# Kernel tuning notes

Measured on AMD Instinct MI355X. Metric: run time of the kernel, lower is better.

## Reference

```python
import jax, jax.numpy as jnp
import numpy as np

N0, N1, N2 = 100000, 300000, 150000
P = 2
DIM = 64


def spmm(rows, cols, vals, dense, n_rows):
    # sparse[n_rows, n_cols] @ dense[n_cols, d] via gather + segment_sum
    return jax.ops.segment_sum(vals[:, None] * dense[cols], rows, num_segments=n_rows)


def powcat(X, p):
    # torch.cat([X**1, ..., X**p], dim=1)
    return jnp.concatenate([X ** n for n in range(1, p + 1)], axis=1)


def setup_inputs() -> dict:
    key = jax.random.key(0)
    ks = iter(jax.random.split(key, 64))

    def randn(shape, scale=1.0):
        return jax.random.normal(next(ks), shape, dtype=jnp.float32) * scale

    def sparse(nr, nc, nnz):
        r = jax.random.randint(next(ks), (nnz,), 0, nr, dtype=jnp.int32)
        c = jax.random.randint(next(ks), (nnz,), 0, nc, dtype=jnp.int32)
        v = randn((nnz,), 0.1)
        return r, c, v

    inp = {}
    inp["X0"] = randn((N0, DIM))
    inp["X1"] = randn((N1, DIM))
    inp["X2"] = randn((N2, DIM))
    for name, nr, nc, nnz in [
        ("L0", N0, N0, 1000000),
        ("L1", N1, N1, 2400000),
        ("L2", N2, N2, 1200000),
        ("D1invB1", N0, N1, 600000),
        ("D2B1TD1inv", N1, N0, 600000),
        ("B2TD2inv", N2, N1, 450000),
        ("B2D3", N1, N2, 450000),
    ]:
        r, c, v = sparse(nr, nc, nnz)
        inp[name + "_rows"], inp[name + "_cols"], inp[name + "_vals"] = r, c, v
    wscale = 1.0 / np.sqrt(DIM * P)
    for name in ["n2n", "n2e", "e2e", "e2n", "e2t", "t2e", "t2t"]:
        inp["W_" + name] = randn((DIM * P, DIM), wscale)
        inp["b_" + name] = randn((DIM,), wscale)
    return inp


def reference(X0, X1, X2,
              L0_rows, L0_cols, L0_vals,
              L1_rows, L1_cols, L1_vals,
              L2_rows, L2_cols, L2_vals,
              D1invB1_rows, D1invB1_cols, D1invB1_vals,
              D2B1TD1inv_rows, D2B1TD1inv_cols, D2B1TD1inv_vals,
              B2TD2inv_rows, B2TD2inv_cols, B2TD2inv_vals,
              B2D3_rows, B2D3_cols, B2D3_vals,
              W_n2n, b_n2n, W_n2e, b_n2e, W_e2e, b_e2e, W_e2n, b_e2n,
              W_e2t, b_e2t, W_t2e, b_t2e, W_t2t, b_t2t):
    X0c = powcat(X0, P)  # [N0, 2*d]
    X1c = powcat(X1, P)  # [N1, 2*d]
    X2c = powcat(X2, P)  # [N2, 2*d]

    n2n = spmm(L0_rows, L0_cols, L0_vals, X0c @ W_n2n + b_n2n, N0)
    n2e = spmm(D2B1TD1inv_rows, D2B1TD1inv_cols, D2B1TD1inv_vals, X0c @ W_n2e + b_n2e, N1)
    e2n = spmm(D1invB1_rows, D1invB1_cols, D1invB1_vals, X1c @ W_e2n + b_e2n, N0)
    e2e = spmm(L1_rows, L1_cols, L1_vals, X1c @ W_e2e + b_e2e, N1)
    e2t = spmm(B2TD2inv_rows, B2TD2inv_cols, B2TD2inv_vals, X1c @ W_e2t + b_e2t, N2)
    t2t = spmm(L2_rows, L2_cols, L2_vals, X2c @ W_t2t + b_t2t, N2)
    t2e = spmm(B2D3_rows, B2D3_cols, B2D3_vals, X2c @ W_t2e + b_t2e, N1)

    Y0 = 0.5 * jax.nn.relu(n2n + e2n)
    Y1 = (1.0 / 3.0) * jax.nn.relu(e2e + n2e + t2e)
    Y2 = 0.5 * jax.nn.relu(t2t + e2t)
    return (Y0, Y1, Y2)
```

## Files before the change

### kernel.cpp

```cpp
#include <hip/hip_runtime.h>
#include <hip/hip_bf16.h>


#define RPB 128
#define COL_MASK 0x7FFFFu
#define LROW_SH 19
#define DID_SH 26
#define CCOL_MASK 0x1FFFFFu
#define CLROW_SH 21
#define CBKT_SH 28
#define MAXNB 4352
#define GBK 4
#define GSH 2
#define NBIN 512
#define MAXNG 1088
#define GRID_BIN 256
#define SPMM_GRID 2048

#define CAPS        15744
#define SORT_PH     8192
#define SORT_LOG    13
#define SORT_MAXBIN 7552
#define MAXPH 16

typedef __attribute__((ext_vector_type(8))) short short8;
typedef __attribute__((ext_vector_type(4))) float f32x4;

__device__ __forceinline__ int   ntld_i(const int* p)   { return __builtin_nontemporal_load(p); }
__device__ __forceinline__ float ntld_f(const float* p) { return __builtin_nontemporal_load(p); }
__device__ __forceinline__ float4 ntld_f4(const float* p) {
    const unsigned long long* q = (const unsigned long long*)p;
    unsigned long long a = __builtin_nontemporal_load(q);
    unsigned long long b = __builtin_nontemporal_load(q + 1);
    float4 v;
    v.x = __uint_as_float((unsigned)a);
    v.y = __uint_as_float((unsigned)(a >> 32));
    v.z = __uint_as_float((unsigned)b);
    v.w = __uint_as_float((unsigned)(b >> 32));
    return v;
}
__device__ __forceinline__ void ntst_f4(float* p, float4 v) {
    unsigned long long a = (unsigned long long)__float_as_uint(v.x)
                         | ((unsigned long long)__float_as_uint(v.y) << 32);
    unsigned long long b = (unsigned long long)__float_as_uint(v.z)
                         | ((unsigned long long)__float_as_uint(v.w) << 32);
    unsigned long long* q = (unsigned long long*)p;
    __builtin_nontemporal_store(a, q);
    __builtin_nontemporal_store(b, q + 1);
}

__device__ __forceinline__ unsigned short f2bf(float f) {
    unsigned u = __float_as_uint(f);
    unsigned r = u + 0x7FFFu + ((u >> 16) & 1u);
    return (unsigned short)(r >> 16);
}

__device__ __forceinline__ void split8(float4 a0, float4 a1, short8& hi, short8& lo) {
    float v[8] = {a0.x, a0.y, a0.z, a0.w, a1.x, a1.y, a1.z, a1.w};
    #pragma unroll
    for (int e = 0; e < 8; ++e) {
        unsigned short h = f2bf(v[e]);
        float hf = __uint_as_float((unsigned)h << 16);
        hi[e] = (short)h;
        lo[e] = (short)f2bf(v[e] - hf);
    }
}

struct WAll { const float* w[7]; };

__global__ __launch_bounds__(256) void winit(WAll wa, unsigned short* __restrict__ frags)
{
    const int s = blockIdx.x;
    const float* __restrict__ W = wa.w[s];
    unsigned short* __restrict__ out = frags + (size_t)s * 16384;
    for (int slot = threadIdx.x; slot < 1024; slot += 256) {
        const int l  = slot & 63;
        const int nf = (slot >> 6) & 3;
        const int kk = slot >> 8;
        const int col = nf * 16 + (l & 15);
        const int kb  = kk * 32 + 8 * (l >> 4);
        short8 vh, vl;
        #pragma unroll
        for (int e = 0; e < 8; ++e) {
            float w = W[(size_t)(kb + e) * 64 + col];
            unsigned short h = f2bf(w);
            float hf = __uint_as_float((unsigned)h << 16);
            vh[e] = (short)h;
            vl[e] = (short)f2bf(w - hf);
        }
        *(short8*)(out + ((size_t)((kk * 4 + nf) * 2 + 0) * 64 + l) * 8) = vh;
        *(short8*)(out + ((size_t)((kk * 4 + nf) * 2 + 1) * 64 + l) * 8) = vl;
    }
}

__device__ __forceinline__ void mfma_set(
    const short8 Ah[4], const short8 Al[4],
    const unsigned short* __restrict__ F, const float* __restrict__ bias,
    unsigned short* __restrict__ D, int nrows, int row0w, int l)
{
    const int lg = l >> 4, lr = l & 15;
    const short8* __restrict__ Fv = (const short8*)F;
    f32x4 acc[4];
    #pragma unroll
    for (int nf = 0; nf < 4; ++nf) {
        float b = bias[nf * 16 + lr];
        f32x4 bi = {b, b, b, b};
        acc[nf] = bi;
    }
    #pragma unroll
    for (int kk = 0; kk < 4; ++kk) {
        #pragma unroll
        for (int nf = 0; nf < 4; ++nf) {
            short8 bh = Fv[((kk * 4 + nf) * 2 + 0) * 64 + l];
            short8 bl = Fv[((kk * 4 + nf) * 2 + 1) * 64 + l];
            acc[nf] = __builtin_amdgcn_mfma_f32_16x16x32_bf16(Ah[kk], bh, acc[nf], 0, 0, 0);
            acc[nf] = __builtin_amdgcn_mfma_f32_16x16x32_bf16(Al[kk], bh, acc[nf], 0, 0, 0);
            acc[nf] = __builtin_amdgcn_mfma_f32_16x16x32_bf16(Ah[kk], bl, acc[nf], 0, 0, 0);
        }
    }
    #pragma unroll
    for (int nf = 0; nf < 4; ++nf) {
        #pragma unroll
        for (int j = 0; j < 4; ++j) {
            int row = row0w + lg * 4 + j;
            if (row < nrows)
                D[(size_t)row * 64 + nf * 16 + lr] = f2bf(acc[nf][j]);
        }
    }
}

__device__ __forceinline__ void gemm_body(
    const float* __restrict__ X, int nrows, int nsets, int row0,
    const unsigned short* F0, const float* b0, unsigned short* D0,
    const unsigned short* F1, const float* b1, unsigned short* D1,
    const unsigned short* F2, const float* b2, unsigned short* D2,
    float Xs[64][68])
{
    const int tid = threadIdx.x;
    #pragma unroll
    for (int it = 0; it < 4; ++it) {
        int idx = tid + it * 256;
        int r = idx >> 4, c4 = idx & 15;
        float4 v = make_float4(0.f, 0.f, 0.f, 0.f);
        if (row0 + r < nrows)
            v = ntld_f4(X + (size_t)(row0 + r) * 64 + c4 * 4);
        *(float4*)&Xs[r][c4 * 4] = v;
    }
    __syncthreads();

    const int w = tid >> 6, l = tid & 63;
    const int lg = l >> 4, lr = l & 15;

    short8 Ah[4], Al[4];
    #pragma unroll
    for (int kk = 0; kk < 4; ++kk) {
        const float* p = &Xs[w * 16 + lr][(kk & 1) * 32 + 8 * lg];
        float4 a0 = *(const float4*)p;
        float4 a1 = *(const float4*)(p + 4);
        if (kk >= 2) {
            a0.x *= a0.x; a0.y *= a0.y; a0.z *= a0.z; a0.w *= a0.w;
            a1.x *= a1.x; a1.y *= a1.y; a1.z *= a1.z; a1.w *= a1.w;
        }
        split8(a0, a1, Ah[kk], Al[kk]);
    }

    const int row0w = row0 + w * 16;
    mfma_set(Ah, Al, F0, b0, D0, nrows, row0w, l);
    if (nsets > 1) mfma_set(Ah, Al, F1, b1, D1, nrows, row0w, l);
    if (nsets > 2) mfma_set(Ah, Al, F2, b2, D2, nrows, row0w, l);
}

__global__ __launch_bounds__(256) void gemm_powcat_mfma(
    const float* __restrict__ X, int nrows, int nsets,
    const unsigned short* __restrict__ F0, const float* __restrict__ b0, unsigned short* __restrict__ D0,
    const unsigned short* __restrict__ F1, const float* __restrict__ b1, unsigned short* __restrict__ D1,
    const unsigned short* __restrict__ F2, const float* __restrict__ b2, unsigned short* __restrict__ D2)
{
    __shared__ float Xs[64][68];
    gemm_body(X, nrows, nsets, blockIdx.x * 64,
              F0, b0, D0, F1, b1, D1, F2, b2, D2, Xs);
}

struct GemmJob {
    const float* X[3];
    const unsigned short* F[9];
    const float* bias[9];
    unsigned short* D[9];
    int nrows[3];
    int nsets[3];
    int blk0[4];
};

__global__ __launch_bounds__(256) void gemm_powcat_all(GemmJob J)
{
    __shared__ float Xs[64][68];
    const int bid = blockIdx.x;
    const int s = (bid >= J.blk0[1] ? 1 : 0) + (bid >= J.blk0[2] ? 1 : 0);
    const int row0 = (bid - J.blk0[s]) * 64;
    gemm_body(J.X[s], J.nrows[s], J.nsets[s], row0,
              J.F[s*3+0], J.bias[s*3+0], J.D[s*3+0],
              J.F[s*3+1], J.bias[s*3+1], J.D[s*3+1],
              J.F[s*3+2], J.bias[s*3+2], J.D[s*3+2], Xs);
}

struct Bin7 {
    const int *r0, *r1, *r2, *r3, *r4, *r5, *r6;
    const int *c0, *c1, *c2, *c3, *c4, *c5, *c6;
    const float *v0, *v1, *v2, *v3, *v4, *v5, *v6;
    int p1, p2, p3, p4, p5, p6, p7;
    int t0, t1, t2, t3, t4, t5, t6;
};

struct CBase { int b[8]; };

struct Ent { int r; int tb; unsigned cw; float v; };

template<bool FULL>
__device__ __forceinline__ Ent decode(const Bin7& B, int i) {
    Ent e;
    if (i < B.p1) {
        int li = i;
        e.r = ntld_i(B.r0 + li); e.tb = B.t0;
        if (FULL) { e.cw = (unsigned)ntld_i(B.c0 + li) | (0u << DID_SH); e.v = ntld_f(B.v0 + li); }
    } else if (i < B.p2) {
        int li = i - B.p1;
        e.r = ntld_i(B.r1 + li); e.tb = B.t1;
        if (FULL) { e.cw = (unsigned)ntld_i(B.c1 + li) | (1u << DID_SH); e.v = ntld_f(B.v1 + li); }
    } else if (i < B.p3) {
        int li = i - B.p2;
        e.r = ntld_i(B.r2 + li); e.tb = B.t2;
        if (FULL) { e.cw = (unsigned)ntld_i(B.c2 + li) | (2u << DID_SH); e.v = ntld_f(B.v2 + li); }
    } else if (i < B.p4) {
        int li = i - B.p3;
        e.r = ntld_i(B.r3 + li); e.tb = B.t3;
        if (FULL) { e.cw = (unsigned)ntld_i(B.c3 + li) | (3u << DID_SH); e.v = ntld_f(B.v3 + li); }
    } else if (i < B.p5) {
        int li = i - B.p4;
        e.r = ntld_i(B.r4 + li); e.tb = B.t4;
        if (FULL) { e.cw = (unsigned)ntld_i(B.c4 + li) | (4u << DID_SH); e.v = ntld_f(B.v4 + li); }
    } else if (i < B.p6) {
        int li = i - B.p5;
        e.r = ntld_i(B.r5 + li); e.tb = B.t5;
        if (FULL) { e.cw = (unsigned)ntld_i(B.c5 + li) | (5u << DID_SH); e.v = ntld_f(B.v5 + li); }
    } else {
        int li = i - B.p6;
        e.r = ntld_i(B.r6 + li); e.tb = B.t6;
        if (FULL) { e.cw = (unsigned)ntld_i(B.c6 + li) | (6u << DID_SH); e.v = ntld_f(B.v6 + li); }
    }
    return e;
}

__global__ __launch_bounds__(1024) void bhist_grp(
    Bin7 B, int* __restrict__ gcount, int* __restrict__ ghist,
    int NG, int chunk)
{
    __shared__ int h[MAXNG];
    for (int i = threadIdx.x; i < NG; i += 1024) h[i] = 0;
    __syncthreads();
    const int s = blockIdx.x * chunk;
    int e = s + chunk;  if (e > B.p7) e = B.p7;
    for (int i = s + threadIdx.x; i < e; i += 1024) {
        Ent en = decode<false>(B, i);
        atomicAdd(&h[(en.tb + (en.r >> 7)) >> GSH], 1);
    }
    __syncthreads();
    for (int i = threadIdx.x; i < NG; i += 1024) {
        int c = h[i];
        ghist[(size_t)blockIdx.x * NG + i] = c;
        if (c) atomicAdd(&gcount[i], c);
    }
}

__global__ __launch_bounds__(1024) void scatter_grpC(
    Bin7 B, CBase cb, int* __restrict__ gcur, const int* __restrict__ ghist,
    uint2* __restrict__ payA, int NG, int chunk)
{
    __shared__ int lbase[MAXNG];
    __shared__ int lcur[MAXNG];
    __shared__ int cbs[8];
    if (threadIdx.x < 8) cbs[threadIdx.x] = cb.b[threadIdx.x];
    for (int i = threadIdx.x; i < NG; i += 1024) {
        int c = ghist[(size_t)blockIdx.x * NG + i];
        lbase[i] = c ? atomicAdd(&gcur[i], c) : 0;
        lcur[i] = 0;
    }
    __syncthreads();
    const int s = blockIdx.x * chunk;
    int e = s + chunk;  if (e > B.p7) e = B.p7;
    for (int i = s + threadIdx.x; i < e; i += 1024) {
        Ent en = decode<true>(B, i);
        int b = en.tb + (en.r >> 7);
        int g = b >> GSH;
        int pos = lbase[g] + atomicAdd(&lcur[g], 1);
        int did = (int)(en.cw >> DID_SH);
        unsigned colC = (en.cw & COL_MASK) + (unsigned)cbs[did];
        unsigned cwA = colC | ((unsigned)(en.r & 127) << CLROW_SH)
                     | ((unsigned)(b & (GBK - 1)) << CBKT_SH);
        payA[pos] = make_uint2(cwA, __float_as_uint(en.v));
    }
}

__global__ __launch_bounds__(1024) void sort_grpC(
    const uint2* __restrict__ payA, const int* __restrict__ goff,
    const int* __restrict__ gcur, int* __restrict__ rowoff,
    int* __restrict__ bend, uint2* __restrict__ payB,
    unsigned char* __restrict__ rowperm, int NBtot)
{
    __shared__ uint2 lpay[CAPS];
    __shared__ unsigned short sidx[CAPS];
    __shared__ int cnt[NBIN];
    __shared__ int off[NBIN];
    __shared__ unsigned char cnts8[NBIN];
    __shared__ int wsum[8];
    __shared__ int phstart[MAXPH + 1];
    __shared__ int s_nph, s_maxbin;

    const int g = blockIdx.x;
    const int tid = threadIdx.x;
    const int seg0 = goff[g], seg1 = gcur[g];
    const int n = seg1 - seg0;
    const bool fast = (n <= CAPS);

    if (tid < NBIN) cnt[tid] = 0;
    if (tid == 0) s_maxbin = 0;
    __syncthreads();
    for (int i = seg0 + tid; i < seg1; i += 1024) {
        unsigned long long pv = __builtin_nontemporal_load(
            (const unsigned long long*)(payA + i));
        unsigned w = (unsigned)pv;
        if (fast) lpay[i - seg0] = make_uint2(w, (unsigned)(pv >> 32));
        atomicAdd(&cnt[(w >> CLROW_SH) & (NBIN - 1)], 1);
    }
    __syncthreads();

    const int lane = tid & 63, wv = tid >> 6;
    const int tot = (tid < NBIN) ? cnt[tid] : 0;
    if (tid < NBIN) {
        atomicMax(&s_maxbin, tot);
        cnts8[tid] = (unsigned char)(tot > 255 ? 255 : tot);
    }
    int x = tot;
    #pragma unroll
    for (int o = 1; o < 64; o <<= 1) {
        int y = __shfl_up(x, o);
        if (lane >= o) x += y;
    }
    if (lane == 63 && wv < 8) wsum[wv] = x;
    __syncthreads();
    if (tid == 0) {
        int acc = 0;
        #pragma unroll
        for (int j = 0; j < 8; ++j) { int t = wsum[j]; wsum[j] = acc; acc += t; }
    }
    __syncthreads();
    int excl = 0;
    if (tid < NBIN) {
        excl = (x - tot) + wsum[wv];
        off[tid] = excl;
        rowoff[(size_t)g * NBIN + tid] = seg0 + excl;
        int b = g * GBK + (tid >> 7);
        if (b < NBtot && (tid & 127) == 127) bend[b] = seg0 + excl + tot;
    }
    __syncthreads();
    if (tid < NBIN) {
        cnt[tid] = excl;
        int p = excl >> SORT_LOG;
        int pprev = (tid == 0) ? -1 : (off[tid - 1] >> SORT_LOG);
        for (int q = pprev + 1; q <= p && q <= MAXPH; ++q) phstart[q] = excl;
        if (tid == NBIN - 1) s_nph = p + 1;
        const int myr = tid & 127, b0 = tid & ~127;
        const unsigned char myc = cnts8[tid];
        int rank = 0;
        #pragma unroll 8
        for (int r = 0; r < 128; ++r) {
            unsigned char c = cnts8[b0 + r];
            rank += (c > myc) || (c == myc && r < myr);
        }
        rowperm[(size_t)g * NBIN + b0 + rank] = (unsigned char)myr;
    }
    __syncthreads();

    if (n <= 0) return;

    if (fast) {
        for (int i = tid; i < n; i += 1024) {
            int bin = (int)(lpay[i].x >> CLROW_SH) & (NBIN - 1);
            int pos = atomicAdd(&cnt[bin], 1);
            sidx[pos] = (unsigned short)i;
        }
        __syncthreads();
        for (int k = tid; k < n; k += 1024) {
            uint2 pv = lpay[sidx[k]];
            unsigned long long o2 = (unsigned long long)(pv.x & CCOL_MASK)
                                  | ((unsigned long long)pv.y << 32);
            __builtin_nontemporal_store(o2,
                (unsigned long long*)(payB + seg0 + k));
        }
    } else if (s_maxbin <= SORT_MAXBIN && s_nph <= MAXPH) {
        const int nph = s_nph;
        for (int ph = 0; ph < nph; ++ph) {
            const int ps = phstart[ph];
            const int pe = (ph + 1 < nph) ? phstart[ph + 1] : n;
            for (int i = seg0 + tid; i < seg1; i += 1024) {
                unsigned long long pv = __builtin_nontemporal_load(
                    (const unsigned long long*)(payA + i));
                unsigned w = (unsigned)pv;
                int bin = (w >> CLROW_SH) & (NBIN - 1);
                if ((off[bin] >> SORT_LOG) == ph) {
                    int pos = atomicAdd(&cnt[bin], 1);
                    lpay[pos - ps] = make_uint2(w, (unsigned)(pv >> 32));
                }
            }
            __syncthreads();
            for (int k = tid; k < pe - ps; k += 1024) {
                uint2 pv = lpay[k];
                unsigned long long o2 = (unsigned long long)(pv.x & CCOL_MASK)
                                      | ((unsigned long long)pv.y << 32);
                __builtin_nontemporal_store(o2,
                    (unsigned long long*)(payB + seg0 + ps + k));
            }
            __syncthreads();
        }
    } else {
        for (int i = seg0 + tid; i < seg1; i += 1024) {
            unsigned long long pv = __builtin_nontemporal_load(
                (const unsigned long long*)(payA + i));
            unsigned w = (unsigned)pv;
            int bin = (w >> CLROW_SH) & (NBIN - 1);
            int pos = seg0 + atomicAdd(&cnt[bin], 1);
            payB[pos] = make_uint2(w & CCOL_MASK, (unsigned)(pv >> 32));
        }
    }
}

__global__ __launch_bounds__(1024) void scatter_grp(
    Bin7 B, int* __restrict__ gcur, const int* __restrict__ ghist,
    uint2* __restrict__ payA, int NG, int chunk)
{
    __shared__ int lbase[MAXNG];
    __shared__ int lcur[MAXNG];
    for (int i = threadIdx.x; i < NG; i += 1024) {
        int c = ghist[(size_t)blockIdx.x * NG + i];
        lbase[i] = c ? atomicAdd(&gcur[i], c) : 0;
        lcur[i] = 0;
    }
    __syncthreads();
    const int s = blockIdx.x * chunk;
    int e = s + chunk;  if (e > B.p7) e = B.p7;
    for (int i = s + threadIdx.x; i < e; i += 1024) {
        Ent en = decode<true>(B, i);
        int b = en.tb + (en.r >> 7);
        int g = b >> GSH;
        int pos = lbase[g] + atomicAdd(&lcur[g], 1);
        unsigned col = en.cw & COL_MASK;
        unsigned did = en.cw >> DID_SH;
        unsigned cwA = col | ((unsigned)(en.r & 127) << LROW_SH)
                     | ((unsigned)(b & (GBK - 1)) << 26) | (did << 29);
        payA[pos] = make_uint2(cwA, __float_as_uint(en.v));
    }
}

__global__ __launch_bounds__(1024) void sort_grp(
    const uint2* __restrict__ payA, const int* __restrict__ goff,
    const int* __restrict__ gcur, int* __restrict__ rowoff,
    int* __restrict__ bend, uint2* __restrict__ payB,
    unsigned char* __restrict__ rowperm, int NBtot)
{
    __shared__ uint2 lpay[CAPS];
    __shared__ unsigned short sidx[CAPS];
    __shared__ int cnt[NBIN];
    __shared__ int off[NBIN];
    __shared__ unsigned char cnts8[NBIN];
    __shared__ int wsum[8];
    __shared__ int phstart[MAXPH + 1];
    __shared__ int s_nph, s_maxbin;

    const int g = blockIdx.x;
    const int tid = threadIdx.x;
    const int seg0 = goff[g], seg1 = gcur[g];
    const int n = seg1 - seg0;
    const bool fast = (n <= CAPS);

    if (tid < NBIN) cnt[tid] = 0;
    if (tid == 0) s_maxbin = 0;
    __syncthreads();
    for (int i = seg0 + tid; i < seg1; i += 1024) {
        unsigned long long pv = __builtin_nontemporal_load(
            (const unsigned long long*)(payA + i));
        unsigned w = (unsigned)pv;
        if (fast) lpay[i - seg0] = make_uint2(w, (unsigned)(pv >> 32));
        atomicAdd(&cnt[(w >> 19) & (NBIN - 1)], 1);
    }
    __syncthreads();

    const int lane = tid & 63, wv = tid >> 6;
    const int tot = (tid < NBIN) ? cnt[tid] : 0;
    if (tid < NBIN) {
        atomicMax(&s_maxbin, tot);
        cnts8[tid] = (unsigned char)(tot > 255 ? 255 : tot);
    }
    int x = tot;
    #pragma unroll
    for (int o = 1; o < 64; o <<= 1) {
        int y = __shfl_up(x, o);
        if (lane >= o) x += y;
    }
    if (lane == 63 && wv < 8) wsum[wv] = x;
    __syncthreads();
    if (tid == 0) {
        int acc = 0;
        #pragma unroll
        for (int j = 0; j < 8; ++j) { int t = wsum[j]; wsum[j] = acc; acc += t; }
    }
    __syncthreads();
    int excl = 0;
    if (tid < NBIN) {
        excl = (x - tot) + wsum[wv];
        off[tid] = excl;
        rowoff[(size_t)g * NBIN + tid] = seg0 + excl;
        int b = g * GBK + (tid >> 7);
        if (b < NBtot && (tid & 127) == 127) bend[b] = seg0 + excl + tot;
    }
    __syncthreads();
    if (tid < NBIN) {
        cnt[tid] = excl;
        int p = excl >> SORT_LOG;
        int pprev = (tid == 0) ? -1 : (off[tid - 1] >> SORT_LOG);
        for (int q = pprev + 1; q <= p && q <= MAXPH; ++q) phstart[q] = excl;
        if (tid == NBIN - 1) s_nph = p + 1;
        const int myr = tid & 127, b0 = tid & ~127;
        const unsigned char myc = cnts8[tid];
        int rank = 0;
        #pragma unroll 8
        for (int r = 0; r < 128; ++r) {
            unsigned char c = cnts8[b0 + r];
            rank += (c > myc) || (c == myc && r < myr);
        }
        rowperm[(size_t)g * NBIN + b0 + rank] = (unsigned char)myr;
    }
    __syncthreads();

    if (n <= 0) return;

    if (fast) {
        for (int i = tid; i < n; i += 1024) {
            int bin = (int)(lpay[i].x >> 19) & (NBIN - 1);
            int pos = atomicAdd(&cnt[bin], 1);
            sidx[pos] = (unsigned short)i;
        }
        __syncthreads();
        for (int k = tid; k < n; k += 1024) {
            uint2 pv = lpay[sidx[k]];
            unsigned cw = (pv.x & 0x03FFFFFFu) | ((pv.x >> 29) << 26);
            unsigned long long o2 = (unsigned long long)cw
                                  | ((unsigned long long)pv.y << 32);
            __builtin_nontemporal_store(o2,
                (unsigned long long*)(payB + seg0 + k));
        }
    } else if (s_maxbin <= SORT_MAXBIN && s_nph <= MAXPH) {
        const int nph = s_nph;
        for (int ph = 0; ph < nph; ++ph) {
            const int ps = phstart[ph];
            const int pe = (ph + 1 < nph) ? phstart[ph + 1] : n;
            for (int i = seg0 + tid; i < seg1; i += 1024) {
                unsigned long long pv = __builtin_nontemporal_load(
                    (const unsigned long long*)(payA + i));
                unsigned w = (unsigned)pv;
                int bin = (w >> 19) & (NBIN - 1);
                if ((off[bin] >> SORT_LOG) == ph) {
                    int pos = atomicAdd(&cnt[bin], 1);
                    lpay[pos - ps] = make_uint2(w, (unsigned)(pv >> 32));
                }
            }
            __syncthreads();
            for (int k = tid; k < pe - ps; k += 1024) {
                uint2 pv = lpay[k];
                unsigned cw = (pv.x & 0x03FFFFFFu) | ((pv.x >> 29) << 26);
                unsigned long long o2 = (unsigned long long)cw
                                      | ((unsigned long long)pv.y << 32);
                __builtin_nontemporal_store(o2,
                    (unsigned long long*)(payB + seg0 + ps + k));
            }
            __syncthreads();
        }
    } else {
        for (int i = seg0 + tid; i < seg1; i += 1024) {
            unsigned long long pv = __builtin_nontemporal_load(
                (const unsigned long long*)(payA + i));
            unsigned w = (unsigned)pv;
            int bin = (w >> 19) & (NBIN - 1);
            int pos = seg0 + atomicAdd(&cnt[bin], 1);
            unsigned cw = (w & 0x03FFFFFFu) | ((w >> 29) << 26);
            payB[pos] = make_uint2(cw, (unsigned)(pv >> 32));
        }
    }
}

__global__ __launch_bounds__(1024) void scan_small(
    const int* __restrict__ in, int* __restrict__ boff,
    int* __restrict__ bcur, int n)
{
    __shared__ int wsum[16];
    __shared__ int carry;
    const int tid = threadIdx.x, lane = tid & 63, wv = tid >> 6;
    if (tid == 0) carry = 0;
    __syncthreads();
    for (int base = 0; base < n; base += 4096) {
        int i = base + tid * 4;
        int v0 = (i + 0 < n) ? in[i + 0] : 0;
        int v1 = (i + 1 < n) ? in[i + 1] : 0;
        int v2 = (i + 2 < n) ? in[i + 2] : 0;
        int v3 = (i + 3 < n) ? in[i + 3] : 0;
        int tsum = v0 + v1 + v2 + v3;
        int x = tsum;
        #pragma unroll
        for (int off = 1; off < 64; off <<= 1) {
            int y = __shfl_up(x, off);
            if (lane >= off) x += y;
        }
        if (lane == 63) wsum[wv] = x;
        int c0 = carry;
        __syncthreads();
        if (tid < 16) {
            int ss = wsum[tid];
            #pragma unroll
            for (int off = 1; off < 16; off <<= 1) {
                int y = __shfl_up(ss, off, 16);
                if (tid >= off) ss += y;
            }
            wsum[tid] = ss;
        }
        __syncthreads();
        int wpre = (wv == 0) ? 0 : wsum[wv - 1];
        int excl = c0 + wpre + (x - tsum);
        if (i + 0 < n) { boff[i + 0] = excl; bcur[i + 0] = excl; } excl += v0;
        if (i + 1 < n) { boff[i + 1] = excl; bcur[i + 1] = excl; } excl += v1;
        if (i + 2 < n) { boff[i + 2] = excl; bcur[i + 2] = excl; } excl += v2;
        if (i + 3 < n) { boff[i + 3] = excl; bcur[i + 3] = excl; }
        __syncthreads();
        if (tid == 0) carry = c0 + wsum[15];
        __syncthreads();
    }
}

__device__ __forceinline__ void facc8(float4& alo, float4& ahi, float v, uint4 d) {
    alo.x = fmaf(v, __uint_as_float((d.x & 0xFFFFu) << 16), alo.x);
    alo.y = fmaf(v, __uint_as_float(d.x & 0xFFFF0000u), alo.y);
    alo.z = fmaf(v, __uint_as_float((d.y & 0xFFFFu) << 16), alo.z);
    alo.w = fmaf(v, __uint_as_float(d.y & 0xFFFF0000u), alo.w);
    ahi.x = fmaf(v, __uint_as_float((d.z & 0xFFFFu) << 16), ahi.x);
    ahi.y = fmaf(v, __uint_as_float(d.z & 0xFFFF0000u), ahi.y);
    ahi.z = fmaf(v, __uint_as_float((d.w & 0xFFFFu) << 16), ahi.z);
    ahi.w = fmaf(v, __uint_as_float(d.w & 0xFFFF0000u), ahi.w);
}

__device__ __forceinline__ void row_accumC8(
    const uint2* __restrict__ payB, int js, int je,
    const uint4* __restrict__ Dg, int l8, float4& alo, float4& ahi)
{
    alo = make_float4(0.f, 0.f, 0.f, 0.f);
    ahi = make_float4(0.f, 0.f, 0.f, 0.f);
    const int n = je - js;
    if (n <= 0) return;
    const uint2* base = payB + js;
    uint2 p0 = base[0];
    uint2 p1 = base[(n > 1) ? 1 : 0];
    float v0 = __uint_as_float(p0.y);
    float v1 = (n > 1) ? __uint_as_float(p1.y) : 0.f;
    uint4 d0 = Dg[(size_t)p0.x * 8 + l8];
    uint4 d1 = Dg[(size_t)p1.x * 8 + l8];
    int i = 0;
    while (true) {
        int i2 = (i + 2 < n) ? i + 2 : n - 1;
        int i3 = (i + 3 < n) ? i + 3 : n - 1;
        uint2 q0 = base[i2];
        uint2 q1 = base[i3];
        float w0 = (i + 2 < n) ? __uint_as_float(q0.y) : 0.f;
        float w1 = (i + 3 < n) ? __uint_as_float(q1.y) : 0.f;
        uint4 e0 = Dg[(size_t)q0.x * 8 + l8];
        uint4 e1 = Dg[(size_t)q1.x * 8 + l8];
        facc8(alo, ahi, v0, d0);
        facc8(alo, ahi, v1, d1);
        i += 2;
        if (i >= n) break;
        v0 = w0; v1 = w1; d0 = e0; d1 = e1;
    }
}

__global__ __launch_bounds__(256) void spmm_stream_allC(
    const uint2* __restrict__ payB, const int* __restrict__ rowoff,
    const int* __restrict__ bend, const unsigned char* __restrict__ rowperm,
    const unsigned short* __restrict__ dense,
    float* __restrict__ out, int NB0, int NB01, int NBall,
    int N0, int N1, int N2)
{
    const uint4* __restrict__ Dg = reinterpret_cast<const uint4*>(dense);
    const int tid = threadIdx.x;
    const int slot = tid >> 3;
    const int l8 = tid & 7;

    for (int t = blockIdx.x; t < NBall; t += gridDim.x) {
        int tb, nrows; float scale; float* oseg;
        if (t < NB0)       { tb = 0;    nrows = N0; oseg = out;                          scale = 0.5f; }
        else if (t < NB01) { tb = NB0;  nrows = N1; oseg = out + (size_t)N0 * 64;        scale = 1.0f / 3.0f; }
        else               { tb = NB01; nrows = N2; oseg = out + (size_t)(N0 + N1) * 64; scale = 0.5f; }
        const int row0 = (t - tb) * RPB;
        const int rbase = t * RPB;
        const int bendt = bend[t];
        const unsigned char* perm = rowperm + (size_t)t * RPB;

        #pragma unroll 1
        for (int rr = 0; rr < 4; ++rr) {
            const int lr = perm[rr * 32 + slot];
            const int row = row0 + lr;
            const int js = rowoff[rbase + lr];
            const int je = (lr == 127) ? bendt : rowoff[rbase + lr + 1];
            float4 alo, ahi;
            row_accumC8(payB, js, je, Dg, l8, alo, ahi);
            if (row < nrows) {
                float* o = oseg + (size_t)row * 64 + l8 * 8;
                alo.x = fmaxf(alo.x, 0.f) * scale;
                alo.y = fmaxf(alo.y, 0.f) * scale;
                alo.z = fmaxf(alo.z, 0.f) * scale;
                alo.w = fmaxf(alo.w, 0.f) * scale;
                ahi.x = fmaxf(ahi.x, 0.f) * scale;
                ahi.y = fmaxf(ahi.y, 0.f) * scale;
                ahi.z = fmaxf(ahi.z, 0.f) * scale;
                ahi.w = fmaxf(ahi.w, 0.f) * scale;
                ntst_f4(o, alo);
                ntst_f4(o + 4, ahi);
            }
        }
    }
}

__device__ __forceinline__ void facc(float4& a, float v, uint2 d) {
    a.x = fmaf(v, __uint_as_float((d.x & 0xFFFFu) << 16), a.x);
    a.y = fmaf(v, __uint_as_float(d.x & 0xFFFF0000u), a.y);
    a.z = fmaf(v, __uint_as_float((d.y & 0xFFFFu) << 16), a.z);
    a.w = fmaf(v, __uint_as_float(d.y & 0xFFFF0000u), a.w);
}

__device__ __forceinline__ float mval(uint2 p, int didMask) {
    int did = (int)(p.x >> DID_SH) & 7;
    return ((didMask >> did) & 1) ? __uint_as_float(p.y) : 0.f;
}
__device__ __forceinline__ uint2 dgather(uint2 p, int l,
    const unsigned short* const* dptr)
{
    const uint2* Dg = reinterpret_cast<const uint2*>(dptr[(p.x >> DID_SH) & 7]);
    return Dg[(size_t)(p.x & COL_MASK) * 16 + l];
}

__device__ __forceinline__ float4 row_accum(
    const uint2* __restrict__ payB, int js, int je,
    const unsigned short* const* dptr, int l, int didMask)
{
    float4 a = make_float4(0.f, 0.f, 0.f, 0.f);
    const int n = je - js;
    if (n <= 0) return a;
    const uint2* base = payB + js;
    uint2 p0 = base[0];
    uint2 p1 = base[(n > 1) ? 1 : 0];
    float v0 = mval(p0, didMask);
    float v1 = (n > 1) ? mval(p1, didMask) : 0.f;
    uint2 d0 = dgather(p0, l, dptr);
    uint2 d1 = dgather(p1, l, dptr);
    int i = 0;
    while (true) {
        int i2 = (i + 2 < n) ? i + 2 : n - 1;
        int i3 = (i + 3 < n) ? i + 3 : n - 1;
        uint2 q0 = base[i2];
        uint2 q1 = base[i3];
        float w0 = (i + 2 < n) ? mval(q0, didMask) : 0.f;
        float w1 = (i + 3 < n) ? mval(q1, didMask) : 0.f;
        uint2 e0 = dgather(q0, l, dptr);
        uint2 e1 = dgather(q1, l, dptr);
        facc(a, v0, d0);
        facc(a, v1, d1);
        i += 2;
        if (i >= n) break;
        v0 = w0; v1 = w1; d0 = e0; d1 = e1;
    }
    return a;
}

__global__ __launch_bounds__(256) void spmm_stream7(
    const uint2* __restrict__ payB, const int* __restrict__ rowoff,
    const int* __restrict__ bend, const unsigned char* __restrict__ rowperm,
    const unsigned short* __restrict__ d0, const unsigned short* __restrict__ d1,
    const unsigned short* __restrict__ d2, const unsigned short* __restrict__ d3,
    const unsigned short* __restrict__ d4, const unsigned short* __restrict__ d5,
    const unsigned short* __restrict__ d6,
    float* __restrict__ out, int tile0, int nrows,
    int firstWrite, int doRelu, float scale, int didMask)
{
    __shared__ const unsigned short* dptr[8];
    const int tid = threadIdx.x;
    if (tid < 8) {
        const unsigned short* tbl[8] = {d0, d1, d2, d3, d4, d5, d6, d0};
        dptr[tid] = tbl[tid];
    }
    __syncthreads();

    const int t = tile0 + blockIdx.x;
    const int qw = tid >> 4, l = tid & 15;
    const int row0 = blockIdx.x * RPB;
    const int rbase = t * RPB;
    const int bendt = bend[t];
    const unsigned char* perm = rowperm + (size_t)t * RPB;

    #pragma unroll 1
    for (int rr = 0; rr < 8; ++rr) {
        const int lr = perm[rr * 16 + qw];
        const int row = row0 + lr;
        const int js = rowoff[rbase + lr];
        const int je = (lr == 127) ? bendt : rowoff[rbase + lr + 1];
        float4 a = row_accum(payB, js, je, dptr, l, didMask);

        if (row < nrows) {
            float* o = out + (size_t)row * 64 + l * 4;
            if (!firstWrite) {
                float4 cur = *reinterpret_cast<float4*>(o);
                a.x += cur.x; a.y += cur.y; a.z += cur.z; a.w += cur.w;
            }
            if (doRelu) {
                a.x = fmaxf(a.x, 0.f) * scale;
                a.y = fmaxf(a.y, 0.f) * scale;
                a.z = fmaxf(a.z, 0.f) * scale;
                a.w = fmaxf(a.w, 0.f) * scale;
            }
            ntst_f4(o, a);
        }
    }
}

extern "C" void kernel_launch(void* const* d_in, const int* in_sizes, int n_in,
                              void* d_out, int out_size, void* d_ws, size_t ws_size,
                              hipStream_t stream)
{
    const float* X0 = (const float*)d_in[0];
    const float* X1 = (const float*)d_in[1];
    const float* X2 = (const float*)d_in[2];
    const int N0 = in_sizes[0] / 64;
    const int N1 = in_sizes[1] / 64;
    const int N2 = in_sizes[2] / 64;

    auto Wp = [&](int i) { return (const float*)d_in[24 + 2 * i]; };
    auto bp = [&](int i) { return (const float*)d_in[25 + 2 * i]; };
    auto Sr = [&](int i) { return (const int*)d_in[3 + 3 * i]; };
    auto Sc = [&](int i) { return (const int*)d_in[4 + 3 * i]; };
    auto Sv = [&](int i) { return (const float*)d_in[5 + 3 * i]; };
    auto Sn = [&](int i) { return in_sizes[3 + 3 * i]; };

    const size_t offY1 = (size_t)N0 * 64;
    const size_t offY2 = (size_t)(N0 + N1) * 64;
    const float TH = 1.0f / 3.0f;

    const int NB0 = (N0 + RPB - 1) / RPB;
    const int NB1 = (N1 + RPB - 1) / RPB;
    const int NB2 = (N2 + RPB - 1) / RPB;

    float* out = (float*)d_out;
    auto align256 = [](size_t x) { return (x + 255) & ~(size_t)255; };

    const size_t FRAG_SET = 16384;
    const size_t fragB = align256(7 * FRAG_SET * sizeof(unsigned short));
    if (ws_size <= fragB) return;
    unsigned short* wfrags = (unsigned short*)d_ws;
    char* ws = (char*)d_ws + fragB;
    const size_t ws_avail = ws_size - fragB;
    auto wf = [&](int i) { return wfrags + (size_t)i * FRAG_SET; };

    WAll wa;
    for (int i = 0; i < 7; ++i) wa.w[i] = Wp(i);
    winit<<<7, 256, 0, stream>>>(wa, wfrags);

    const int NBall = NB0 + NB1 + NB2;
    const int NGall = (NBall + GBK - 1) / GBK;
    const int nnzAll = Sn(0)+Sn(1)+Sn(2)+Sn(3)+Sn(4)+Sn(5)+Sn(6);
    const size_t payT1 = align256((size_t)nnzAll * sizeof(uint2));
    const size_t cntT1 = align256((size_t)(NBall + 8) * sizeof(int));
    const size_t rowT1 = align256((size_t)NGall * NBIN * sizeof(int));
    const size_t permT1 = align256((size_t)NGall * NBIN);
    const size_t ghT1 = align256((size_t)GRID_BIN * NGall * sizeof(int));
    const size_t denseT1 = ((size_t)2*N0 + 3*N1 + 2*N2) * 64 * sizeof(unsigned short);
    const size_t regionT1 = denseT1 > payT1 ? denseT1 : payT1;
    const size_t needT1 = payT1 + 4 * cntT1 + rowT1 + permT1 + ghT1 + regionT1;
    const long long denseRows = (long long)2*N0 + 3LL*N1 + 2LL*N2;

    if (ws_avail >= needT1 && NBall <= MAXNB && denseRows < (1LL << 21)) {
        uint2* payB  = (uint2*)ws;
        int* goff    = (int*)(ws + payT1);
        int* gcur    = (int*)(ws + payT1 + 1 * cntT1);
        int* bend    = (int*)(ws + payT1 + 2 * cntT1);
        int* gcount  = (int*)(ws + payT1 + 3 * cntT1);
        int* rowoff  = (int*)(ws + payT1 + 4 * cntT1);
        unsigned char* rowperm = (unsigned char*)(ws + payT1 + 4 * cntT1 + rowT1);
        int* ghist   = (int*)(ws + payT1 + 4 * cntT1 + rowT1 + permT1);
        char* region = ws + payT1 + 4 * cntT1 + rowT1 + permT1 + ghT1;
        uint2* payA  = (uint2*)region;
        unsigned short* db = (unsigned short*)region;
        unsigned short* dn2n = db;
        unsigned short* de2n = dn2n + (size_t)N0 * 64;
        unsigned short* dn2e = de2n + (size_t)N1 * 64;
        unsigned short* de2e = dn2e + (size_t)N0 * 64;
        unsigned short* dt2e = de2e + (size_t)N1 * 64;
        unsigned short* de2t = dt2e + (size_t)N2 * 64;
        unsigned short* dt2t = de2t + (size_t)N1 * 64;

        Bin7 B;
        B.r0 = Sr(0); B.c0 = Sc(0); B.v0 = Sv(0);
        B.r1 = Sr(3); B.c1 = Sc(3); B.v1 = Sv(3);
        B.r2 = Sr(4); B.c2 = Sc(4); B.v2 = Sv(4);
        B.r3 = Sr(1); B.c3 = Sc(1); B.v3 = Sv(1);
        B.r4 = Sr(6); B.c4 = Sc(6); B.v4 = Sv(6);
        B.r5 = Sr(5); B.c5 = Sc(5); B.v5 = Sv(5);
        B.r6 = Sr(2); B.c6 = Sc(2); B.v6 = Sv(2);
        B.p1 = Sn(0);
        B.p2 = B.p1 + Sn(3);
        B.p3 = B.p2 + Sn(4);
        B.p4 = B.p3 + Sn(1);
        B.p5 = B.p4 + Sn(6);
        B.p6 = B.p5 + Sn(5);
        B.p7 = B.p6 + Sn(2);
        B.t0 = 0;   B.t1 = 0;
        B.t2 = NB0; B.t3 = NB0; B.t4 = NB0;
        B.t5 = NB0 + NB1; B.t6 = NB0 + NB1;

        CBase cb;
        cb.b[0] = 0;
        cb.b[1] = N0;
        cb.b[2] = N0 + N1;
        cb.b[3] = 2*N0 + N1;
        cb.b[4] = 2*N0 + 2*N1;
        cb.b[5] = 2*N0 + 2*N1 + N2;
        cb.b[6] = 2*N0 + 3*N1 + N2;
        cb.b[7] = 0;

        const int chunk = (B.p7 + GRID_BIN - 1) / GRID_BIN;
        hipMemsetAsync(gcount, 0, (size_t)NGall * sizeof(int), stream);
        bhist_grp<<<GRID_BIN, 1024, 0, stream>>>(B, gcount, ghist, NGall, chunk);
        scan_small<<<1, 1024, 0, stream>>>(gcount, goff, gcur, NGall);
        scatter_grpC<<<GRID_BIN, 1024, 0, stream>>>(B, cb, gcur, ghist, payA,
                                                    NGall, chunk);
        sort_grpC<<<NGall, 1024, 0, stream>>>(payA, goff, gcur, rowoff, bend,
                                              payB, rowperm, NBall);

        GemmJob J;
        J.X[0] = X0; J.X[1] = X1; J.X[2] = X2;
        J.nrows[0] = N0; J.nrows[1] = N1; J.nrows[2] = N2;
        J.nsets[0] = 2;  J.nsets[1] = 3;  J.nsets[2] = 2;
        J.F[0] = wf(0); J.bias[0] = bp(0); J.D[0] = dn2n;
        J.F[1] = wf(1); J.bias[1] = bp(1); J.D[1] = dn2e;
        J.F[2] = wf(0); J.bias[2] = bp(0); J.D[2] = dn2n;
        J.F[3] = wf(3); J.bias[3] = bp(3); J.D[3] = de2n;
        J.F[4] = wf(2); J.bias[4] = bp(2); J.D[4] = de2e;
        J.F[5] = wf(4); J.bias[5] = bp(4); J.D[5] = de2t;
        J.F[6] = wf(5); J.bias[6] = bp(5); J.D[6] = dt2e;
        J.F[7] = wf(6); J.bias[7] = bp(6); J.D[7] = dt2t;
        J.F[8] = wf(5); J.bias[8] = bp(5); J.D[8] = dt2e;
        const int gb0 = (N0 + 63) / 64, gb1 = (N1 + 63) / 64, gb2 = (N2 + 63) / 64;
        J.blk0[0] = 0; J.blk0[1] = gb0; J.blk0[2] = gb0 + gb1;
        J.blk0[3] = gb0 + gb1 + gb2;
        gemm_powcat_all<<<J.blk0[3], 256, 0, stream>>>(J);

        const int grid = NBall < SPMM_GRID ? NBall : SPMM_GRID;
        spmm_stream_allC<<<grid, 256, 0, stream>>>(payB, rowoff, bend, rowperm,
            db, out, NB0, NB0 + NB1, NBall, N0, N1, N2);
        return;
    }

    const int NBtotA = NB0 + NB2;
    const int NBmax = NBtotA > NB1 ? NBtotA : NB1;
    const int NGmax = (NBmax + GBK - 1) / GBK;
    const int nnzA = Sn(0) + Sn(3) + Sn(5) + Sn(2);
    const int nnzB = Sn(4) + Sn(6) + Sn(1);
    const int nnzMax = nnzA > nnzB ? nnzA : nnzB;

    const size_t payBsz = align256((size_t)nnzMax * sizeof(uint2));
    const size_t cntB = align256((size_t)(NBmax + 8) * sizeof(int));
    const size_t rowB = align256((size_t)NGmax * NBIN * sizeof(int));
    const size_t permB = align256((size_t)NGmax * NBIN);
    const size_t ghB = align256((size_t)GRID_BIN * NGmax * sizeof(int));
    const size_t denseOff = payBsz + 4 * cntB + rowB + permB + ghB;

    uint2* bpayB = (uint2*)ws;
    int* goff    = (int*)(ws + payBsz);
    int* gcur    = (int*)(ws + payBsz + 1 * cntB);
    int* bend    = (int*)(ws + payBsz + 2 * cntB);
    int* gcount  = (int*)(ws + payBsz + 3 * cntB);
    int* rowoff  = (int*)(ws + payBsz + 4 * cntB);
    unsigned char* rowperm = (unsigned char*)(ws + payBsz + 4 * cntB + rowB);
    int* ghist   = (int*)(ws + payBsz + 4 * cntB + rowB + permB);
    unsigned short* dense = (unsigned short*)(ws + denseOff);
    uint2* payA  = (uint2*)dense;

    const size_t need_full = denseOff +
        ((size_t)N0 + N2 + N1) * 64 * sizeof(unsigned short);
    const bool fullB = (ws_avail >= need_full);

    {
        Bin7 B;
        B.r0 = Sr(0); B.c0 = Sc(0); B.v0 = Sv(0);
        B.r1 = Sr(3); B.c1 = Sc(3); B.v1 = Sv(3);
        B.r2 = Sr(5); B.c2 = Sc(5); B.v2 = Sv(5);
        B.r3 = Sr(2); B.c3 = Sc(2); B.v3 = Sv(2);
        B.r4 = B.r3; B.c4 = B.c3; B.v4 = B.v3;
        B.r5 = B.r3; B.c5 = B.c3; B.v5 = B.v3;
        B.r6 = B.r3; B.c6 = B.c3; B.v6 = B.v3;
        B.p1 = Sn(0);
        B.p2 = B.p1 + Sn(3);
        B.p3 = B.p2 + Sn(5);
        B.p4 = B.p3 + Sn(2);
        B.p5 = B.p4; B.p6 = B.p4; B.p7 = B.p4;
        B.t0 = 0; B.t1 = 0; B.t2 = NB0; B.t3 = NB0;
        B.t4 = NB0; B.t5 = NB0; B.t6 = NB0;

        const int NGA = (NBtotA + GBK - 1) / GBK;
        const int chunk = (B.p7 + GRID_BIN - 1) / GRID_BIN;
        hipMemsetAsync(gcount, 0, (size_t)NGA * sizeof(int), stream);
        bhist_grp<<<GRID_BIN, 1024, 0, stream>>>(B, gcount, ghist, NGA, chunk);
        scan_small<<<1, 1024, 0, stream>>>(gcount, goff, gcur, NGA);
        scatter_grp<<<GRID_BIN, 1024, 0, stream>>>(B, gcur, ghist, payA, NGA, chunk);
        sort_grp<<<NGA, 1024, 0, stream>>>(payA, goff, gcur, rowoff, bend,
                                           bpayB, rowperm, NBtotA);

        unsigned short* dn2n = dense;
        unsigned short* de2n = dense + (size_t)N0 * 64;
        gemm_powcat_mfma<<<(N0 + 63) / 64, 256, 0, stream>>>(
            X0, N0, 1, wf(0), bp(0), dn2n,
            wf(0), bp(0), dn2n, wf(0), bp(0), dn2n);
        gemm_powcat_mfma<<<(N1 + 63) / 64, 256, 0, stream>>>(
            X1, N1, 1, wf(3), bp(3), de2n,
            wf(3), bp(3), de2n, wf(3), bp(3), de2n);
        spmm_stream7<<<NB0, 256, 0, stream>>>(bpayB, rowoff, bend, rowperm,
            dn2n, de2n, dn2n, dn2n, dn2n, dn2n, dn2n,
            out, 0, N0, 1, 1, 0.5f, 0x7F);

        unsigned short* de2t = dense;
        unsigned short* dt2t = dense + (size_t)N1 * 64;
        gemm_powcat_mfma<<<(N1 + 63) / 64, 256, 0, stream>>>(
            X1, N1, 1, wf(4), bp(4), de2t,
            wf(4), bp(4), de2t, wf(4), bp(4), de2t);
        gemm_powcat_mfma<<<(N2 + 63) / 64, 256, 0, stream>>>(
            X2, N2, 1, wf(6), bp(6), dt2t,
            wf(6), bp(6), dt2t, wf(6), bp(6), dt2t);
        spmm_stream7<<<NB2, 256, 0, stream>>>(bpayB, rowoff, bend, rowperm,
            de2t, de2t, de2t, dt2t, de2t, de2t, de2t,
            out + offY2, NB0, N2, 1, 1, 0.5f, 0x7F);
    }

    {
        Bin7 B;
        B.r0 = Sr(4); B.c0 = Sc(4); B.v0 = Sv(4);
        B.r1 = Sr(6); B.c1 = Sc(6); B.v1 = Sv(6);
        B.r2 = Sr(1); B.c2 = Sc(1); B.v2 = Sv(1);
        B.r3 = B.r2; B.c3 = B.c2; B.v3 = B.v2;
        B.r4 = B.r2; B.c4 = B.c2; B.v4 = B.v2;
        B.r5 = B.r2; B.c5 = B.c2; B.v5 = B.v2;
        B.r6 = B.r2; B.c6 = B.c2; B.v6 = B.v2;
        B.p1 = Sn(4);
        B.p2 = B.p1 + Sn(6);
        B.p3 = B.p2 + Sn(1);
        B.p4 = B.p3; B.p5 = B.p3; B.p6 = B.p3; B.p7 = B.p3;
        B.t0 = 0; B.t1 = 0; B.t2 = 0; B.t3 = 0; B.t4 = 0; B.t5 = 0; B.t6 = 0;

        const int NGB = (NB1 + GBK - 1) / GBK;
        const int chunk = (B.p7 + GRID_BIN - 1) / GRID_BIN;
        hipMemsetAsync(gcount, 0, (size_t)NGB * sizeof(int), stream);
        bhist_grp<<<GRID_BIN, 1024, 0, stream>>>(B, gcount, ghist, NGB, chunk);
        scan_small<<<1, 1024, 0, stream>>>(gcount, goff, gcur, NGB);
        scatter_grp<<<GRID_BIN, 1024, 0, stream>>>(B, gcur, ghist, payA, NGB, chunk);
        sort_grp<<<NGB, 1024, 0, stream>>>(payA, goff, gcur, rowoff, bend,
                                           bpayB, rowperm, NB1);

        if (fullB) {
            unsigned short* dn2e = dense;
            unsigned short* dt2e = dense + (size_t)N0 * 64;
            unsigned short* de2e = dense + ((size_t)N0 + N2) * 64;
            gemm_powcat_mfma<<<(N0 + 63) / 64, 256, 0, stream>>>(
                X0, N0, 1, wf(1), bp(1), dn2e,
                wf(1), bp(1), dn2e, wf(1), bp(1), dn2e);
            gemm_powcat_mfma<<<(N2 + 63) / 64, 256, 0, stream>>>(
                X2, N2, 1, wf(5), bp(5), dt2e,
                wf(5), bp(5), dt2e, wf(5), bp(5), dt2e);
            gemm_powcat_mfma<<<(N1 + 63) / 64, 256, 0, stream>>>(
                X1, N1, 1, wf(2), bp(2), de2e,
                wf(2), bp(2), de2e, wf(2), bp(2), de2e);
            spmm_stream7<<<NB1, 256, 0, stream>>>(bpayB, rowoff, bend, rowperm,
                dn2e, dt2e, de2e, dn2e, dn2e, dn2e, dn2e,
                out + offY1, 0, N1, 1, 1, TH, 0x7F);
        } else {
            unsigned short* dn2e = dense;
            unsigned short* dt2e = dense + (size_t)N0 * 64;
            gemm_powcat_mfma<<<(N0 + 63) / 64, 256, 0, stream>>>(
                X0, N0, 1, wf(1), bp(1), dn2e,
                wf(1), bp(1), dn2e, wf(1), bp(1), dn2e);
            gemm_powcat_mfma<<<(N2 + 63) / 64, 256, 0, stream>>>(
                X2, N2, 1, wf(5), bp(5), dt2e,
                wf(5), bp(5), dt2e, wf(5), bp(5), dt2e);
            spmm_stream7<<<NB1, 256, 0, stream>>>(bpayB, rowoff, bend, rowperm,
                dn2e, dt2e, dn2e, dn2e, dn2e, dn2e, dn2e,
                out + offY1, 0, N1, 1, 0, 0.f, 0x3);
            unsigned short* de2e = dense;
            gemm_powcat_mfma<<<(N1 + 63) / 64, 256, 0, stream>>>(
                X1, N1, 1, wf(2), bp(2), de2e,
                wf(2), bp(2), de2e, wf(2), bp(2), de2e);
            spmm_stream7<<<NB1, 256, 0, stream>>>(bpayB, rowoff, bend, rowperm,
                de2e, de2e, de2e, de2e, de2e, de2e, de2e,
                out + offY1, 0, N1, 0, 1, TH, 0x4);
        }
    }
}
```

Baseline: 491.7 us.

## Fuse scatter and dense GEMM into one launch to overlap independent work

```diff
diff --git a/kernel.cpp b/kernel.cpp
--- a/kernel.cpp
+++ b/kernel.cpp
@@ -130,13 +130,12 @@
 }
 
 __device__ __forceinline__ void gemm_body(
-    const float* __restrict__ X, int nrows, int nsets, int row0,
+    const float* __restrict__ X, int nrows, int nsets, int row0, int tid,
     const unsigned short* F0, const float* b0, unsigned short* D0,
     const unsigned short* F1, const float* b1, unsigned short* D1,
     const unsigned short* F2, const float* b2, unsigned short* D2,
     float Xs[64][68])
 {
-    const int tid = threadIdx.x;
     #pragma unroll
     for (int it = 0; it < 4; ++it) {
         int idx = tid + it * 256;
@@ -177,7 +176,7 @@
     const unsigned short* __restrict__ F2, const float* __restrict__ b2, unsigned short* __restrict__ D2)
 {
     __shared__ float Xs[64][68];
-    gemm_body(X, nrows, nsets, blockIdx.x * 64,
+    gemm_body(X, nrows, nsets, blockIdx.x * 64, threadIdx.x,
               F0, b0, D0, F1, b1, D1, F2, b2, D2, Xs);
 }
 
@@ -197,7 +196,7 @@
     const int bid = blockIdx.x;
     const int s = (bid >= J.blk0[1] ? 1 : 0) + (bid >= J.blk0[2] ? 1 : 0);
     const int row0 = (bid - J.blk0[s]) * 64;
-    gemm_body(J.X[s], J.nrows[s], J.nsets[s], row0,
+    gemm_body(J.X[s], J.nrows[s], J.nsets[s], row0, threadIdx.x,
               J.F[s*3+0], J.bias[s*3+0], J.D[s*3+0],
               J.F[s*3+1], J.bias[s*3+1], J.D[s*3+1],
               J.F[s*3+2], J.bias[s*3+2], J.D[s*3+2], Xs);
@@ -271,15 +270,14 @@
     }
 }
 
-__global__ __launch_bounds__(1024) void scatter_grpC(
-    Bin7 B, CBase cb, int* __restrict__ gcur, const int* __restrict__ ghist,
-    uint2* __restrict__ payA, int NG, int chunk)
-{
-    __shared__ int lbase[MAXNG];
-    __shared__ int lcur[MAXNG];
-    __shared__ int cbs[8];
-    if (threadIdx.x < 8) cbs[threadIdx.x] = cb.b[threadIdx.x];
-    for (int i = threadIdx.x; i < NG; i += 1024) {
+__device__ __forceinline__ void scatter_bodyC(
+    const Bin7& B, const CBase& cb, int* gcur, const int* ghist,
+    uint2* payA, int NG, int chunk,
+    int* lbase, int* lcur, int* cbs)
+{
+    const int tid = threadIdx.x;
+    if (tid < 8) cbs[tid] = cb.b[tid];
+    for (int i = tid; i < NG; i += 1024) {
         int c = ghist[(size_t)blockIdx.x * NG + i];
         lbase[i] = c ? atomicAdd(&gcur[i], c) : 0;
         lcur[i] = 0;
@@ -287,7 +285,7 @@
     __syncthreads();
     const int s = blockIdx.x * chunk;
     int e = s + chunk;  if (e > B.p7) e = B.p7;
-    for (int i = s + threadIdx.x; i < e; i += 1024) {
+    for (int i = s + tid; i < e; i += 1024) {
         Ent en = decode<true>(B, i);
         int b = en.tb + (en.r >> 7);
         int g = b >> GSH;
@@ -297,6 +295,48 @@
         unsigned cwA = colC | ((unsigned)(en.r & 127) << CLROW_SH)
                      | ((unsigned)(b & (GBK - 1)) << CBKT_SH);
         payA[pos] = make_uint2(cwA, __float_as_uint(en.v));
+    }
+}
+
+__global__ __launch_bounds__(1024) void scatter_grpC(
+    Bin7 B, CBase cb, int* __restrict__ gcur, const int* __restrict__ ghist,
+    uint2* __restrict__ payA, int NG, int chunk)
+{
+    __shared__ int lbase[MAXNG];
+    __shared__ int lcur[MAXNG];
+    __shared__ int cbs[8];
+    scatter_bodyC(B, cb, gcur, ghist, payA, NG, chunk, lbase, lcur, cbs);
+}
+
+struct FusedSG {
+    Bin7 B; CBase cb; GemmJob J;
+    int NG, chunk, nScatter;
+};
+
+__global__ __launch_bounds__(1024, 8) void scatter_gemm_fused(
+    FusedSG F, int* __restrict__ gcur, const int* __restrict__ ghist,
+    uint2* __restrict__ payA)
+{
+    __shared__ float Xs4[4][64][68];
+    __shared__ int lbase[MAXNG];
+    __shared__ int lcur[MAXNG];
+    __shared__ int cbs[8];
+
+    if ((int)blockIdx.x < F.nScatter) {
+        scatter_bodyC(F.B, F.cb, gcur, ghist, payA, F.NG, F.chunk,
+                      lbase, lcur, cbs);
+    } else {
+        const GemmJob& J = F.J;
+        const int tid = threadIdx.x;
+        int gt = (blockIdx.x - F.nScatter) * 4 + (tid >> 8);
+        if (gt >= J.blk0[3]) gt = J.blk0[3] - 1;
+        const int s = (gt >= J.blk0[1] ? 1 : 0) + (gt >= J.blk0[2] ? 1 : 0);
+        const int row0 = (gt - J.blk0[s]) * 64;
+        gemm_body(J.X[s], J.nrows[s], J.nsets[s], row0, tid & 255,
+                  J.F[s*3+0], J.bias[s*3+0], J.D[s*3+0],
+                  J.F[s*3+1], J.bias[s*3+1], J.D[s*3+1],
+                  J.F[s*3+2], J.bias[s*3+2], J.D[s*3+2],
+                  Xs4[tid >> 8]);
     }
 }
 
@@ -884,12 +924,15 @@
     const size_t rowT1 = align256((size_t)NGall * NBIN * sizeof(int));
     const size_t permT1 = align256((size_t)NGall * NBIN);
     const size_t ghT1 = align256((size_t)GRID_BIN * NGall * sizeof(int));
-    const size_t denseT1 = ((size_t)2*N0 + 3*N1 + 2*N2) * 64 * sizeof(unsigned short);
+    const size_t denseT1 = align256(((size_t)2*N0 + 3*N1 + 2*N2) * 64 * sizeof(unsigned short));
     const size_t regionT1 = denseT1 > payT1 ? denseT1 : payT1;
-    const size_t needT1 = payT1 + 4 * cntT1 + rowT1 + permT1 + ghT1 + regionT1;
+    const size_t tablesT1 = 4 * cntT1 + rowT1 + permT1 + ghT1;
+    const size_t needT1 = payT1 + tablesT1 + regionT1;
+    const size_t needOV = payT1 + tablesT1 + payT1 + denseT1;
     const long long denseRows = (long long)2*N0 + 3LL*N1 + 2LL*N2;
 
     if (ws_avail >= needT1 && NBall <= MAXNB && denseRows < (1LL << 21)) {
+        const bool overlap = (ws_avail >= needOV);
         uint2* payB  = (uint2*)ws;
         int* goff    = (int*)(ws + payT1);
         int* gcur    = (int*)(ws + payT1 + 1 * cntT1);
@@ -898,9 +941,10 @@
         int* rowoff  = (int*)(ws + payT1 + 4 * cntT1);
         unsigned char* rowperm = (unsigned char*)(ws + payT1 + 4 * cntT1 + rowT1);
         int* ghist   = (int*)(ws + payT1 + 4 * cntT1 + rowT1 + permT1);
-        char* region = ws + payT1 + 4 * cntT1 + rowT1 + permT1 + ghT1;
+        char* region = ws + payT1 + tablesT1;
         uint2* payA  = (uint2*)region;
-        unsigned short* db = (unsigned short*)region;
+        unsigned short* db = overlap ? (unsigned short*)(region + payT1)
+                                     : (unsigned short*)region;
         unsigned short* dn2n = db;
         unsigned short* de2n = dn2n + (size_t)N0 * 64;
         unsigned short* dn2e = de2n + (size_t)N1 * 64;
@@ -938,15 +982,6 @@
         cb.b[6] = 2*N0 + 3*N1 + N2;
         cb.b[7] = 0;
 
-        const int chunk = (B.p7 + GRID_BIN - 1) / GRID_BIN;
-        hipMemsetAsync(gcount, 0, (size_t)NGall * sizeof(int), stream);
-        bhist_grp<<<GRID_BIN, 1024, 0, stream>>>(B, gcount, ghist, NGall, chunk);
-        scan_small<<<1, 1024, 0, stream>>>(gcount, goff, gcur, NGall);
-        scatter_grpC<<<GRID_BIN, 1024, 0, stream>>>(B, cb, gcur, ghist, payA,
-                                                    NGall, chunk);
-        sort_grpC<<<NGall, 1024, 0, stream>>>(payA, goff, gcur, rowoff, bend,
-                                              payB, rowperm, NBall);
-
         GemmJob J;
         J.X[0] = X0; J.X[1] = X1; J.X[2] = X2;
         J.nrows[0] = N0; J.nrows[1] = N1; J.nrows[2] = N2;
@@ -963,7 +998,28 @@
         const int gb0 = (N0 + 63) / 64, gb1 = (N1 + 63) / 64, gb2 = (N2 + 63) / 64;
         J.blk0[0] = 0; J.blk0[1] = gb0; J.blk0[2] = gb0 + gb1;
         J.blk0[3] = gb0 + gb1 + gb2;
-        gemm_powcat_all<<<J.blk0[3], 256, 0, stream>>>(J);
+
+        const int chunk = (B.p7 + GRID_BIN - 1) / GRID_BIN;
+        hipMemsetAsync(gcount, 0, (size_t)NGall * sizeof(int), stream);
+        bhist_grp<<<GRID_BIN, 1024, 0, stream>>>(B, gcount, ghist, NGall, chunk);
+        scan_small<<<1, 1024, 0, stream>>>(gcount, goff, gcur, NGall);
+
+        if (overlap) {
+            FusedSG F;
+            F.B = B; F.cb = cb; F.J = J;
+            F.NG = NGall; F.chunk = chunk; F.nScatter = GRID_BIN;
+            const int nGemmBlk = (J.blk0[3] + 3) / 4;
+            scatter_gemm_fused<<<GRID_BIN + nGemmBlk, 1024, 0, stream>>>(
+                F, gcur, ghist, payA);
+            sort_grpC<<<NGall, 1024, 0, stream>>>(payA, goff, gcur, rowoff,
+                                                  bend, payB, rowperm, NBall);
+        } else {
+            scatter_grpC<<<GRID_BIN, 1024, 0, stream>>>(B, cb, gcur, ghist,
+                                                        payA, NGall, chunk);
+            sort_grpC<<<NGall, 1024, 0, stream>>>(payA, goff, gcur, rowoff,
+                                                  bend, payB, rowperm, NBall);
+            gemm_powcat_all<<<J.blk0[3], 256, 0, stream>>>(J);
+        }
 
         const int grid = NBall < SPMM_GRID ? NBall : SPMM_GRID;
         spmm_stream_allC<<<grid, 256, 0, stream>>>(payB, rowoff, bend, rowperm,
```

Result: slower. 727.1 us (+47.9%).
